# Performance work log

Hardware: AMD Instinct MI355X
Metric: run time of the kernel (lower is better)

Reference implementation:

```python
import jax, jax.numpy as jnp
import numpy as np

B, C_IN, H, W = 4, 256, 64, 64
LATENT = 256


def conv1x1(x, w, b):
    # x: [B, Cin, H, W], w: [Cout, Cin], b: [Cout]
    return jnp.einsum('bchw,oc->bohw', x, w) + b[None, :, None, None]


def setup_inputs() -> dict:
    key = jax.random.key(0)
    ks = jax.random.split(key, 9)
    s_in = 1.0 / np.sqrt(C_IN)
    s_lat = 1.0 / np.sqrt(LATENT)
    return {
        'x': jax.random.normal(ks[0], (B, C_IN, H, W), dtype=jnp.float32),
        'Wq': jax.random.normal(ks[1], (LATENT, C_IN), dtype=jnp.float32) * s_in,
        'bq': jax.random.normal(ks[2], (LATENT,), dtype=jnp.float32) * 0.01,
        'Wk': jax.random.normal(ks[3], (LATENT, C_IN), dtype=jnp.float32) * s_in,
        'bk': jax.random.normal(ks[4], (LATENT,), dtype=jnp.float32) * 0.01,
        'Wv': jax.random.normal(ks[5], (LATENT, C_IN), dtype=jnp.float32) * s_in,
        'bv': jax.random.normal(ks[6], (LATENT,), dtype=jnp.float32) * 0.01,
        'Wo': jax.random.normal(ks[7], (C_IN, LATENT), dtype=jnp.float32) * s_lat,
        'bo': jax.random.normal(ks[8], (C_IN,), dtype=jnp.float32) * 0.01,
    }


def reference(x, Wq, bq, Wk, bk, Wv, bv, Wo, bo):
    b, _, h, w = x.shape
    n = h * w
    q = conv1x1(x, Wq, bq).reshape(b, LATENT, n)  # [B, L, N]
    k = conv1x1(x, Wk, bk).reshape(b, LATENT, n)
    v = conv1x1(x, Wv, bv).reshape(b, LATENT, n)
    scale = jnp.sqrt(jnp.asarray(LATENT, dtype=x.dtype))
    # attention[b, i, j] = sum_c q[b, c, i] * k[b, c, j]
    attn = jnp.einsum('bci,bcj->bij', q, k) / scale
    # faithful to original: softmax over dim=1 (query index i, per column j)
    attn = jax.nn.softmax(attn, axis=1)
    # res[b, c, j] = sum_i v[b, c, i] * attn[b, i, j]
    res = jnp.einsum('bci,bij->bcj', v, attn).reshape(b, LATENT, h, w)
    return conv1x1(res, Wo, bo)
```

## Files before the change

kernel.cpp:

```cpp
#include <hip/hip_runtime.h>

#define B_  4
#define C_  256
#define N_  4096
#define SCALE 0.0625f

typedef short s8v __attribute__((ext_vector_type(8)));
typedef float f4v __attribute__((ext_vector_type(4)));

static __device__ __forceinline__ ushort f2bf(float f) {
  union { float f; uint u; } v; v.f = f;
  return (ushort)((v.u + 0x7FFFu + ((v.u >> 16) & 1u)) >> 16);
}

static __device__ __forceinline__ void gload_lds16(const ushort* g, ushort* l) {
  __builtin_amdgcn_global_load_lds(
      (const __attribute__((address_space(1))) void*)g,
      (__attribute__((address_space(3))) void*)l, 16, 0, 0);
}

__global__ __launch_bounds__(256) void xpose_cast(
    const float* __restrict__ x, ushort* __restrict__ x_t,
    float* __restrict__ den)
{
  const int b  = blockIdx.z;
  const int c0 = blockIdx.y * 64;
  const int n0 = blockIdx.x * 64;
  __shared__ float t[64][65];

  if (blockIdx.y == 0 && threadIdx.x < 64)
    den[b * N_ + n0 + threadIdx.x] = 0.f;

  const int tc = threadIdx.x >> 4;
  const int tn = (threadIdx.x & 15) * 4;
  #pragma unroll
  for (int cc = 0; cc < 64; cc += 16) {
    float4 v = *(const float4*)(x + (size_t)(b * C_ + c0 + cc + tc) * N_ + n0 + tn);
    t[cc + tc][tn + 0] = v.x;
    t[cc + tc][tn + 1] = v.y;
    t[cc + tc][tn + 2] = v.z;
    t[cc + tc][tn + 3] = v.w;
  }
  __syncthreads();

  const int on = threadIdx.x >> 2;
  const int oc = (threadIdx.x & 3) * 16;
  union { ushort us[16]; uint4 q[2]; } o;
  #pragma unroll
  for (int i = 0; i < 16; ++i) o.us[i] = f2bf(t[oc + i][on]);
  ushort* dst = x_t + (size_t)(b * N_ + n0 + on) * C_ + c0 + oc;
  *(uint4*)dst       = o.q[0];
  *(uint4*)(dst + 8) = o.q[1];
}

__global__ __launch_bounds__(256, 2) void qkv_mfma(
    const ushort* __restrict__ x_t,
    const float* __restrict__ Wq, const float* __restrict__ bq,
    const float* __restrict__ Wk, const float* __restrict__ bk,
    const float* __restrict__ Wv, const float* __restrict__ bv,
    ushort* __restrict__ q_t, ushort* __restrict__ k_t, ushort* __restrict__ v_bf)
{
  const int p = blockIdx.z >> 2;
  const int b = blockIdx.z & 3;
  const float* W  = (p == 0) ? Wq : (p == 1) ? Wk : Wv;
  const float* bi = (p == 0) ? bq : (p == 1) ? bk : bv;
  const int l0    = blockIdx.y * 64;
  const int nseg  = blockIdx.x * 512;

  const int tid  = threadIdx.x;
  const int lane = tid & 63;
  const int wave = tid >> 6;
  const int l16  = lane & 15;
  const int quad = lane >> 4;

  __shared__ __align__(16) ushort w_lds[64 * 264];
  __shared__ __align__(16) ushort x_lds[64 * 264];

  for (int g = tid; g < 4096; g += 256) {
    int row = g >> 6, col4 = (g & 63) * 4;
    float4 wv = *(const float4*)(W + (size_t)(l0 + row) * 256 + col4);
    *(ushort4*)&w_lds[row * 264 + col4] =
        make_ushort4(f2bf(wv.x), f2bf(wv.y), f2bf(wv.z), f2bf(wv.w));
  }
  __syncthreads();

  s8v kw[4][8];
  #pragma unroll
  for (int lt = 0; lt < 4; ++lt)
    #pragma unroll
    for (int cs = 0; cs < 8; ++cs)
      kw[lt][cs] = *(const s8v*)&w_lds[(lt * 16 + l16) * 264 + quad * 8 + cs * 32];

  float bias_l[4];
  #pragma unroll
  for (int lt = 0; lt < 4; ++lt) bias_l[lt] = bi[l0 + lt * 16 + l16];

  for (int it = 0; it < 8; ++it) {
    const int n0 = nseg + it * 64;
    {
      const ushort* xseg = x_t + (size_t)(b * N_ + n0) * C_;
      #pragma unroll
      for (int k = 0; k < 8; ++k) {
        int c = tid + k * 256;
        uint4 d = *(const uint4*)(xseg + (size_t)c * 8);
        *(uint4*)&x_lds[(c >> 5) * 264 + (c & 31) * 8] = d;
      }
    }
    __syncthreads();

    f4v s[4];
    #pragma unroll
    for (int lt = 0; lt < 4; ++lt) s[lt] = (f4v){0.f, 0.f, 0.f, 0.f};
    const ushort* xa_base = x_lds + (wave * 16 + l16) * 264 + quad * 8;
    #pragma unroll
    for (int cs = 0; cs < 8; ++cs) {
      s8v xa = *(const s8v*)(xa_base + cs * 32);
      #pragma unroll
      for (int lt = 0; lt < 4; ++lt)
        s[lt] = __builtin_amdgcn_mfma_f32_16x16x32_bf16(xa, kw[lt][cs], s[lt], 0, 0, 0);
    }

    const int nb = n0 + wave * 16 + quad * 4;
    if (p < 2) {
      ushort* outp = (p == 0) ? q_t : k_t;
      #pragma unroll
      for (int lt = 0; lt < 4; ++lt) {
        const int l = l0 + lt * 16 + l16;
        #pragma unroll
        for (int r = 0; r < 4; ++r)
          outp[(size_t)(b * N_ + nb + r) * C_ + l] = f2bf(s[lt][r] + bias_l[lt]);
      }
    } else {
      #pragma unroll
      for (int lt = 0; lt < 4; ++lt) {
        const int c_out = l0 + lt * 16 + l16;
        *(ushort4*)&v_bf[(size_t)(b * C_ + c_out) * N_ + nb] =
            make_ushort4(f2bf(s[lt][0] + bias_l[lt]), f2bf(s[lt][1] + bias_l[lt]),
                         f2bf(s[lt][2] + bias_l[lt]), f2bf(s[lt][3] + bias_l[lt]));
      }
    }
    __syncthreads();
  }
}

__global__ __launch_bounds__(256, 2) void flash8b(
    const ushort* __restrict__ q_t, const ushort* __restrict__ k_t,
    const ushort* __restrict__ v_bf, ushort* __restrict__ res0,
    ushort* __restrict__ res1, float* __restrict__ den)
{
  const int tid  = threadIdx.x;
  const int lane = tid & 63;
  const int wave = tid >> 6;
  const int l16  = lane & 15;
  const int quad = lane >> 4;
  const int jw    = blockIdx.x * 64;
  const int seg   = blockIdx.y;
  const int ibase = seg * 2048;
  const int b     = blockIdx.z;

  const int wqk_j = wave & 1;
  const int wqk_i = wave >> 1;

  __shared__ __align__(16) ushort q_lds[64 * 256];
  __shared__ __align__(16) ushort p_lds[64 * 64];

  s8v kf[2][8];
  #pragma unroll
  for (int jt = 0; jt < 2; ++jt) {
    const ushort* kp = k_t + (size_t)(b * N_ + jw + wqk_j * 32 + jt * 16 + l16) * C_ + quad * 8;
    #pragma unroll
    for (int cs = 0; cs < 8; ++cs) kf[jt][cs] = *(const s8v*)(kp + cs * 32);
  }

  f4v acc[4][4];
  #pragma unroll
  for (int m = 0; m < 4; ++m)
    #pragma unroll
    for (int t = 0; t < 4; ++t) acc[m][t] = (f4v){0.f, 0.f, 0.f, 0.f};
  float dacc0 = 0.f, dacc1 = 0.f;

  const ushort* vbase0 = v_bf + (size_t)(b * C_ + wave * 64 + l16) * N_ + quad * 8;

  for (int it = 0; it < 32; ++it) {
    const int i0 = ibase + it * 64;

    {
      const ushort* qseg = q_t + ((size_t)(b * N_) + i0) * C_;
      const int plo = lane & 31;
      #pragma unroll
      for (int k = 0; k < 8; ++k) {
        const int row = k * 8 + wave * 2 + (lane >> 5);
        const ushort* src = qseg + row * 256 + ((plo ^ (row & 7)) << 3);
        gload_lds16(src, &q_lds[k * 2048 + wave * 512]);
      }
    }

    s8v av[4][2];
    #pragma unroll
    for (int m = 0; m < 4; ++m)
      #pragma unroll
      for (int ks = 0; ks < 2; ++ks)
        av[m][ks] = *(const s8v*)(vbase0 + (size_t)(m * 16) * N_ + i0 + ks * 32);

    __syncthreads();

    #pragma unroll
    for (int itile = 0; itile < 2; ++itile) {
      const int i_loc = (wqk_i * 2 + itile) * 16;
      f4v s0 = (f4v){0.f, 0.f, 0.f, 0.f};
      f4v s1 = (f4v){0.f, 0.f, 0.f, 0.f};
      const int qrow = i_loc + l16;
      const ushort* qa_row = q_lds + qrow * 256;
      const int qsw = qrow & 7;
      __builtin_amdgcn_s_setprio(1);
      #pragma unroll
      for (int cs = 0; cs < 8; ++cs) {
        s8v qa = *(const s8v*)(qa_row + (((quad + 4 * cs) ^ qsw) << 3));
        s0 = __builtin_amdgcn_mfma_f32_16x16x32_bf16(qa, kf[0][cs], s0, 0, 0, 0);
        s1 = __builtin_amdgcn_mfma_f32_16x16x32_bf16(qa, kf[1][cs], s1, 0, 0, 0);
      }
      __builtin_amdgcn_s_setprio(0);
      {
        float e0 = __expf(s0[0] * SCALE), e1 = __expf(s0[1] * SCALE);
        float e2 = __expf(s0[2] * SCALE), e3 = __expf(s0[3] * SCALE);
        dacc0 += (e0 + e1) + (e2 + e3);
        const int row = wqk_j * 32 + l16;
        const int col = i_loc + quad * 4;
        *(ushort4*)&p_lds[row * 64 + ((((col >> 3) ^ (row & 7)) << 3) | (col & 7))] =
            make_ushort4(f2bf(e0), f2bf(e1), f2bf(e2), f2bf(e3));
      }
      {
        float e0 = __expf(s1[0] * SCALE), e1 = __expf(s1[1] * SCALE);
        float e2 = __expf(s1[2] * SCALE), e3 = __expf(s1[3] * SCALE);
        dacc1 += (e0 + e1) + (e2 + e3);
        const int row = wqk_j * 32 + 16 + l16;
        const int col = i_loc + quad * 4;
        *(ushort4*)&p_lds[row * 64 + ((((col >> 3) ^ (row & 7)) << 3) | (col & 7))] =
            make_ushort4(f2bf(e0), f2bf(e1), f2bf(e2), f2bf(e3));
      }
    }

    __syncthreads();

    #pragma unroll
    for (int ks = 0; ks < 2; ++ks) {
      s8v pb[4];
      #pragma unroll
      for (int t = 0; t < 4; ++t) {
        const int row = t * 16 + l16;
        const int col = ks * 32 + quad * 8;
        pb[t] = *(const s8v*)&p_lds[row * 64 + (((col >> 3) ^ (row & 7)) << 3)];
      }
      __builtin_amdgcn_s_setprio(1);
      #pragma unroll
      for (int m = 0; m < 4; ++m)
        #pragma unroll
        for (int t = 0; t < 4; ++t)
          acc[m][t] = __builtin_amdgcn_mfma_f32_16x16x32_bf16(av[m][ks], pb[t], acc[m][t], 0, 0, 0);
      __builtin_amdgcn_s_setprio(0);
    }
  }

  dacc0 += __shfl_xor(dacc0, 16);  dacc0 += __shfl_xor(dacc0, 32);
  dacc1 += __shfl_xor(dacc1, 16);  dacc1 += __shfl_xor(dacc1, 32);
  if (lane < 16) {
    atomicAdd(&den[b * N_ + jw + wqk_j * 32 + lane], dacc0);
    atomicAdd(&den[b * N_ + jw + wqk_j * 32 + 16 + lane], dacc1);
  }

  #pragma unroll
  for (int m = 0; m < 4; ++m) {
    const int c0 = wave * 64 + m * 16 + quad * 4;
    #pragma unroll
    for (int t = 0; t < 4; ++t) {
      const int row = t * 16 + l16;
      *(ushort4*)&q_lds[row * 256 + ((((c0 >> 3) ^ (row & 7)) << 3) | (c0 & 7))] =
          make_ushort4(f2bf(acc[m][t][0]), f2bf(acc[m][t][1]),
                       f2bf(acc[m][t][2]), f2bf(acc[m][t][3]));
    }
  }
  __syncthreads();
  {
    ushort* rp = (seg ? res1 : res0) + (size_t)(b * N_ + jw) * C_;
    #pragma unroll
    for (int k = 0; k < 8; ++k) {
      int c = tid + k * 256;
      int row = c >> 5, ch = c & 31;
      uint4 d = *(const uint4*)&q_lds[row * 256 + ((ch ^ (row & 7)) << 3)];
      *(uint4*)&rp[(size_t)row * C_ + ch * 8] = d;
    }
  }
}

__global__ __launch_bounds__(256, 2) void out_mfma(
    const ushort* __restrict__ res0, const ushort* __restrict__ res1,
    const float* __restrict__ Wo, const float* __restrict__ bo,
    const float* __restrict__ den, float* __restrict__ out)
{
  const int b    = blockIdx.z;
  const int co0  = blockIdx.y * 64;
  const int nseg = blockIdx.x * 256;

  const int tid  = threadIdx.x;
  const int lane = tid & 63;
  const int wave = tid >> 6;
  const int l16  = lane & 15;
  const int quad = lane >> 4;

  __shared__ __align__(16) ushort w_lds[64 * 264];
  __shared__ __align__(16) ushort r_lds[2][64 * 264];

  for (int g = tid; g < 4096; g += 256) {
    int row = g >> 6, col4 = (g & 63) * 4;
    float4 wv = *(const float4*)(Wo + (size_t)(co0 + row) * 256 + col4);
    *(ushort4*)&w_lds[row * 264 + col4] =
        make_ushort4(f2bf(wv.x), f2bf(wv.y), f2bf(wv.z), f2bf(wv.w));
  }
  __syncthreads();

  s8v kw[4][8];
  #pragma unroll
  for (int lt = 0; lt < 4; ++lt)
    #pragma unroll
    for (int cs = 0; cs < 8; ++cs)
      kw[lt][cs] = *(const s8v*)&w_lds[(lt * 16 + l16) * 264 + quad * 8 + cs * 32];

  float bias_l[4];
  #pragma unroll
  for (int lt = 0; lt < 4; ++lt) bias_l[lt] = bo[co0 + lt * 16 + l16];

  for (int it = 0; it < 4; ++it) {
    const int n0 = nseg + it * 64;
    {
      const ushort* r0 = res0 + (size_t)(b * N_ + n0) * C_;
      const ushort* r1 = res1 + (size_t)(b * N_ + n0) * C_;
      #pragma unroll
      for (int k = 0; k < 8; ++k) {
        int c = tid + k * 256;
        uint4 d0 = *(const uint4*)(r0 + (size_t)c * 8);
        uint4 d1 = *(const uint4*)(r1 + (size_t)c * 8);
        *(uint4*)&r_lds[0][(c >> 5) * 264 + (c & 31) * 8] = d0;
        *(uint4*)&r_lds[1][(c >> 5) * 264 + (c & 31) * 8] = d1;
      }
    }
    __syncthreads();

    f4v s[4];
    #pragma unroll
    for (int lt = 0; lt < 4; ++lt) s[lt] = (f4v){0.f, 0.f, 0.f, 0.f};
    #pragma unroll
    for (int buf = 0; buf < 2; ++buf) {
      const ushort* ra_base = r_lds[buf] + (wave * 16 + l16) * 264 + quad * 8;
      #pragma unroll
      for (int cs = 0; cs < 8; ++cs) {
        s8v ra = *(const s8v*)(ra_base + cs * 32);
        #pragma unroll
        for (int lt = 0; lt < 4; ++lt)
          s[lt] = __builtin_amdgcn_mfma_f32_16x16x32_bf16(ra, kw[lt][cs], s[lt], 0, 0, 0);
      }
    }

    const int nb = n0 + wave * 16 + quad * 4;
    float4 dv = *(const float4*)(den + (size_t)b * N_ + nb);
    const float di0 = 1.0f / dv.x, di1 = 1.0f / dv.y, di2 = 1.0f / dv.z, di3 = 1.0f / dv.w;
    #pragma unroll
    for (int lt = 0; lt < 4; ++lt) {
      const int co = co0 + lt * 16 + l16;
      *(float4*)&out[(size_t)(b * C_ + co) * N_ + nb] =
          make_float4(s[lt][0] * di0 + bias_l[lt], s[lt][1] * di1 + bias_l[lt],
                      s[lt][2] * di2 + bias_l[lt], s[lt][3] * di3 + bias_l[lt]);
    }
    __syncthreads();
  }
}

extern "C" void kernel_launch(void* const* d_in, const int* in_sizes, int n_in,
                              void* d_out, int out_size, void* d_ws, size_t ws_size,
                              hipStream_t stream)
{
  const float* x  = (const float*)d_in[0];
  const float* Wq = (const float*)d_in[1];
  const float* bq = (const float*)d_in[2];
  const float* Wk = (const float*)d_in[3];
  const float* bk = (const float*)d_in[4];
  const float* Wv = (const float*)d_in[5];
  const float* bv = (const float*)d_in[6];
  const float* Wo = (const float*)d_in[7];
  const float* bo = (const float*)d_in[8];
  float* out = (float*)d_out;

  char* ws = (char*)d_ws;
  ushort* q_t  = (ushort*)(ws);
  ushort* k_t  = (ushort*)(ws + (size_t)8  * 1024 * 1024);
  ushort* v_bf = (ushort*)(ws + (size_t)16 * 1024 * 1024);
  ushort* res0 = (ushort*)(ws + (size_t)24 * 1024 * 1024);
  ushort* res1 = (ushort*)(ws + (size_t)32 * 1024 * 1024);
  float*  den  = (float*) (ws + (size_t)40 * 1024 * 1024);
  ushort* x_t  = (ushort*)(ws + (size_t)40 * 1024 * 1024 + 65536);

  xpose_cast<<<dim3(64, 4, 4), dim3(256), 0, stream>>>(x, x_t, den);
  qkv_mfma <<<dim3(8, 4, 12),  dim3(256), 0, stream>>>(x_t, Wq, bq, Wk, bk, Wv, bv, q_t, k_t, v_bf);
  flash8b  <<<dim3(64, 2, 4),  dim3(256), 0, stream>>>(q_t, k_t, v_bf, res0, res1, den);
  out_mfma <<<dim3(16, 4, 4),  dim3(256), 0, stream>>>(res0, res1, Wo, bo, den, out);
}
```

Before: 208.1 us.

## Double-buffer Q tiles in LDS with async prefetch of the next tile

The Q shared-memory tile in the flash attention kernel is split into two buffers. The next iteration's Q tile is prefetched with global_load_lds while the current one is consumed. The full __syncthreads calls are replaced by targeted s_waitcnt vmcnt/lgkmcnt plus s_barrier, which lets the V register loads and the next Q load stay in flight across the barrier. This doubles the Q LDS footprint and adds a redundant load on the last iteration, and it relies on hand-counted vmcnt values being correct.

New measurement: 205.1 us. Within noise of the previous version (-1.5%).

```diff
diff --git a/kernel.cpp b/kernel.cpp
--- a/kernel.cpp
+++ b/kernel.cpp
@@ -161,8 +161,11 @@
   const int wqk_j = wave & 1;
   const int wqk_i = wave >> 1;
 
-  __shared__ __align__(16) ushort q_lds[64 * 256];
+  __shared__ __align__(16) ushort q_lds[2][64 * 256];
   __shared__ __align__(16) ushort p_lds[64 * 64];
+
+  const ushort* qseg_b = q_t + (size_t)(b * N_) * C_;
+  const int plo = lane & 31;
 
   s8v kf[2][8];
   #pragma unroll
@@ -172,6 +175,16 @@
     for (int cs = 0; cs < 8; ++cs) kf[jt][cs] = *(const s8v*)(kp + cs * 32);
   }
 
+  {
+    const ushort* qseg = qseg_b + (size_t)ibase * C_;
+    #pragma unroll
+    for (int k = 0; k < 8; ++k) {
+      const int row = k * 8 + wave * 2 + (lane >> 5);
+      gload_lds16(qseg + row * 256 + ((plo ^ (row & 7)) << 3),
+                  &q_lds[0][k * 2048 + wave * 512]);
+    }
+  }
+
   f4v acc[4][4];
   #pragma unroll
   for (int m = 0; m < 4; ++m)
@@ -181,28 +194,37 @@
 
   const ushort* vbase0 = v_bf + (size_t)(b * C_ + wave * 64 + l16) * N_ + quad * 8;
 
+  #pragma unroll 1
   for (int it = 0; it < 32; ++it) {
+    const int cur = it & 1;
     const int i0 = ibase + it * 64;
+    const int inext = (it < 31) ? (it + 1) : 31;
+
+    s8v av[4][2];
+    #pragma unroll
+    for (int m = 0; m < 4; ++m)
+      #pragma unroll
+      for (int ks = 0; ks < 2; ++ks)
+        av[m][ks] = *(const s8v*)(vbase0 + (size_t)(m * 16) * N_ + i0 + ks * 32);
+
+    __builtin_amdgcn_sched_barrier(0);
 
     {
-      const ushort* qseg = q_t + ((size_t)(b * N_) + i0) * C_;
-      const int plo = lane & 31;
+      const ushort* qseg = qseg_b + (size_t)(ibase + inext * 64) * C_;
+      ushort* dstb = &q_lds[cur ^ 1][0];
       #pragma unroll
       for (int k = 0; k < 8; ++k) {
         const int row = k * 8 + wave * 2 + (lane >> 5);
-        const ushort* src = qseg + row * 256 + ((plo ^ (row & 7)) << 3);
-        gload_lds16(src, &q_lds[k * 2048 + wave * 512]);
-      }
-    }
-
-    s8v av[4][2];
-    #pragma unroll
-    for (int m = 0; m < 4; ++m)
-      #pragma unroll
-      for (int ks = 0; ks < 2; ++ks)
-        av[m][ks] = *(const s8v*)(vbase0 + (size_t)(m * 16) * N_ + i0 + ks * 32);
-
-    __syncthreads();
+        gload_lds16(qseg + row * 256 + ((plo ^ (row & 7)) << 3),
+                    dstb + k * 2048 + wave * 512);
+      }
+    }
+
+    __builtin_amdgcn_sched_barrier(0);
+    asm volatile("s_waitcnt vmcnt(16)" ::: "memory");
+    __builtin_amdgcn_sched_barrier(0);
+    __builtin_amdgcn_s_barrier();
+    __builtin_amdgcn_sched_barrier(0);
 
     #pragma unroll
     for (int itile = 0; itile < 2; ++itile) {
@@ -210,7 +232,7 @@
       f4v s0 = (f4v){0.f, 0.f, 0.f, 0.f};
       f4v s1 = (f4v){0.f, 0.f, 0.f, 0.f};
       const int qrow = i_loc + l16;
-      const ushort* qa_row = q_lds + qrow * 256;
+      const ushort* qa_row = &q_lds[cur][0] + qrow * 256;
       const int qsw = qrow & 7;
       __builtin_amdgcn_s_setprio(1);
       #pragma unroll
@@ -240,7 +262,11 @@
       }
     }
 
-    __syncthreads();
+    __builtin_amdgcn_sched_barrier(0);
+    asm volatile("s_waitcnt lgkmcnt(0)" ::: "memory");
+    __builtin_amdgcn_sched_barrier(0);
+    __builtin_amdgcn_s_barrier();
+    __builtin_amdgcn_sched_barrier(0);
 
     #pragma unroll
     for (int ks = 0; ks < 2; ++ks) {
@@ -261,6 +287,8 @@
     }
   }
 
+  __syncthreads();
+
   dacc0 += __shfl_xor(dacc0, 16);  dacc0 += __shfl_xor(dacc0, 32);
   dacc1 += __shfl_xor(dacc1, 16);  dacc1 += __shfl_xor(dacc1, 32);
   if (lane < 16) {
@@ -274,7 +302,7 @@
     #pragma unroll
     for (int t = 0; t < 4; ++t) {
       const int row = t * 16 + l16;
-      *(ushort4*)&q_lds[row * 256 + ((((c0 >> 3) ^ (row & 7)) << 3) | (c0 & 7))] =
+      *(ushort4*)&q_lds[0][row * 256 + ((((c0 >> 3) ^ (row & 7)) << 3) | (c0 & 7))] =
           make_ushort4(f2bf(acc[m][t][0]), f2bf(acc[m][t][1]),
                        f2bf(acc[m][t][2]), f2bf(acc[m][t][3]));
     }
@@ -286,7 +314,7 @@
     for (int k = 0; k < 8; ++k) {
       int c = tid + k * 256;
       int row = c >> 5, ch = c & 31;
-      uint4 d = *(const uint4*)&q_lds[row * 256 + ((ch ^ (row & 7)) << 3)];
+      uint4 d = *(const uint4*)&q_lds[0][row * 256 + ((ch ^ (row & 7)) << 3)];
       *(uint4*)&rp[(size_t)row * C_ + ch * 8] = d;
     }
   }
```
